# Optimization experiments

Hardware: AMD Instinct MI355X
Metric: run time of the kernel (lower is better)

## Reference

```python
import jax, jax.numpy as jnp
from jax import lax
import numpy as np

H, HKV, D = 16, 4, 128          # query heads, kv heads, head dim
ROT_DIM = 128                    # rotary applied to full head dim
BASE = 10000.0


def rope_cos_sin(S, dtype):
    inv_freq = 1.0 / (BASE ** (jnp.arange(0, ROT_DIM, 2, dtype=jnp.float32) / ROT_DIM))
    t = jnp.arange(S, dtype=jnp.float32)
    freqs = jnp.outer(t, inv_freq)          # (S, ROT_DIM//2)
    return jnp.cos(freqs).astype(dtype), jnp.sin(freqs).astype(dtype)


def apply_rope(x, cos, sin):
    # x: (B, S, h, D); non-interleaved (GPT-NeoX) halves
    d2 = ROT_DIM // 2
    x1, x2 = x[..., :d2], x[..., d2:ROT_DIM]
    c = cos[None, :, None, :]
    s = sin[None, :, None, :]
    rot = jnp.concatenate([x1 * c - x2 * s, x2 * c + x1 * s], axis=-1)
    if ROT_DIM < x.shape[-1]:
        rot = jnp.concatenate([rot, x[..., ROT_DIM:]], axis=-1)
    return rot


def setup_inputs() -> dict:
    key = jax.random.key(0)
    ks = jax.random.split(key, 7)
    B, S, E = 2, 2048, 2048
    qkv_dim = D * (H + 2 * HKV)  # 3072
    return {
        "x": jax.random.normal(ks[0], (B, S, E), jnp.float32),
        "w_in": jax.random.normal(ks[1], (qkv_dim, E), jnp.float32) * (1.0 / np.sqrt(E)),
        "b_in": jax.random.normal(ks[2], (qkv_dim,), jnp.float32) * 0.02,
        "conv_w": jax.random.normal(ks[3], (qkv_dim, 1, 4), jnp.float32) * 0.5,
        "conv_b": jax.random.normal(ks[4], (qkv_dim,), jnp.float32) * 0.02,
        "w_out": jax.random.normal(ks[5], (E, H * D), jnp.float32) * (1.0 / np.sqrt(H * D)),
        "b_out": jax.random.normal(ks[6], (E,), jnp.float32) * 0.02,
    }


def reference(x, w_in, b_in, conv_w, conv_b, w_out, b_out):
    B, S, E = x.shape
    K = conv_w.shape[-1]
    # fused QKV projection
    qkv = x @ w_in.T + b_in                                  # (B, S, 3072)
    # causal depthwise conv1d (torch conv with padding=K-1 then keep first S)
    lhs = jnp.pad(qkv.transpose(0, 2, 1), ((0, 0), (0, 0), (K - 1, 0)))  # (B, C, S+K-1)
    conv = lax.conv_general_dilated(
        lhs, conv_w, (1,), "VALID",
        dimension_numbers=("NCH", "OIH", "NCH"),
        feature_group_count=conv_w.shape[0],
    )
    qkv = (conv + conv_b[None, :, None]).transpose(0, 2, 1)  # (B, S, 3072)
    # split q / kv (GQA)
    q = qkv[..., : H * D].reshape(B, S, H, D)
    kv = qkv[..., H * D :].reshape(B, S, 2, HKV, D)
    cos, sin = rope_cos_sin(S, x.dtype)
    q = apply_rope(q, cos, sin)
    k = apply_rope(kv[:, :, 0], cos, sin)
    v = kv[:, :, 1]
    rep = H // HKV
    k = jnp.repeat(k, rep, axis=2)                           # (B, S, H, D)
    v = jnp.repeat(v, rep, axis=2)
    scale = 1.0 / np.sqrt(D)  # softmax_scale=None -> 1/sqrt(head_dim)
    scores = jnp.einsum("bshd,bthd->bhst", q, k) * scale     # (B, H, S, S)
    causal_mask = jnp.tril(jnp.ones((S, S), bool))
    scores = jnp.where(causal_mask[None, None], scores, jnp.finfo(scores.dtype).min)
    attn = jax.nn.softmax(scores, axis=-1)
    ctx = jnp.einsum("bhst,bthd->bshd", attn, v).reshape(B, S, H * D)
    return ctx @ w_out.T + b_out
```

## Files before the change

kernel.cpp:

```cpp
#include <hip/hip_runtime.h>
#include <type_traits>

#define S_LEN 2048
#define BATCH 2
#define EDIM  2048
#define NH    16
#define NKV   4
#define HDIM  128
#define QKVD  3072
#define QSCALE 0.12751579107188777f

typedef __attribute__((ext_vector_type(8))) short short8;
typedef __attribute__((ext_vector_type(4))) float f32x4;

__device__ __forceinline__ ushort f2bf(float f) {
  union { float f; unsigned u; } un; un.f = f;
  unsigned u = un.u + 0x7fffu + ((un.u >> 16) & 1u);
  return (ushort)(u >> 16);
}
__device__ __forceinline__ float bf2f(ushort h) {
  union { unsigned u; float f; } un; un.u = ((unsigned)h) << 16;
  return un.f;
}
__device__ __forceinline__ unsigned cvt_pk_bf16(float lo, float hi) {
  unsigned r;
  asm("v_cvt_pk_bf16_f32 %0, %1, %2" : "=v"(r) : "v"(lo), "v"(hi));
  return r;
}
__device__ __forceinline__ float fexp2(float x) { return __builtin_amdgcn_exp2f(x); }

__device__ __forceinline__ void load_lds16(const void* g, void* l) {
  __builtin_amdgcn_global_load_lds((const __attribute__((address_space(1))) void*)g,
                                   (__attribute__((address_space(3))) void*)l,
                                   16, 0, 0);
}

__global__ __launch_bounds__(256) void cast3(const float* __restrict__ a,
                                             const float* __restrict__ b,
                                             const float* __restrict__ c,
                                             ushort* __restrict__ oa,
                                             ushort* __restrict__ ob,
                                             ushort* __restrict__ oc) {
  int i = blockIdx.x * 256 + threadIdx.x;
  const float* s; ushort* d; int j;
  if (i < 2097152)      { s = a; d = oa; j = i; }
  else if (i < 3670016) { s = b; d = ob; j = i - 2097152; }
  else                  { s = c; d = oc; j = i - 3670016; }
  float4 v = ((const float4*)s)[j];
  ushort4 o;
  o.x = f2bf(v.x); o.y = f2bf(v.y); o.z = f2bf(v.z); o.w = f2bf(v.w);
  ((ushort4*)d)[j] = o;
}

__global__ __launch_bounds__(256) void transpose_cw(const float* __restrict__ cw,
                                                    float* __restrict__ cwT) {
  int i = blockIdx.x * 256 + threadIdx.x;
  int c = i >> 2, j = i & 3;
  cwT[j * QKVD + c] = cw[i];
}

__global__ __launch_bounds__(256) void rope_table(float* __restrict__ cosT,
                                                  float* __restrict__ sinT) {
  int i = blockIdx.x * 256 + threadIdx.x;
  int s = i >> 6, d = i & 63;
  float inv = expf(-(float)d * 0.14391156831212787f);
  float f = (float)s * inv;
  float sv, cv;
  sincosf(f, &sv, &cv);
  cosT[i] = cv;
  sinT[i] = sv;
}

template <bool OBF>
__global__ __launch_bounds__(256) void gemm_bt(
    const ushort* __restrict__ A, const ushort* __restrict__ Bt,
    const float* __restrict__ bias, void* __restrict__ Cv,
    int M, int N, int K) {
  __shared__ __align__(16) ushort As[128 * 32];
  __shared__ __align__(16) ushort Bs[128 * 32];
  const int tid = threadIdx.x;
  const int wid = tid >> 6, lane = tid & 63;
  const int l15 = lane & 15, lg = lane >> 4;
  const int nTn = N >> 7;
  const int cpx = gridDim.x >> 3;
  const int swz = ((int)blockIdx.x & 7) * cpx + ((int)blockIdx.x >> 3);
  const int m0 = (swz / nTn) * 128, n0 = (swz % nTn) * 128;
  const int wr = (wid >> 1) * 64, wc = (wid & 1) * 64;
  f32x4 acc[4][4] = {};

  for (int k0 = 0; k0 < K; k0 += 32) {
#pragma unroll
    for (int j = 0; j < 2; ++j) {
      const int c = j * 256 + wid * 64 + lane;
      load_lds16(A + (size_t)(m0 + (c >> 2)) * K + k0 + (c & 3) * 8,
                 As + (j * 256 + wid * 64) * 8);
      load_lds16(Bt + (size_t)(n0 + (c >> 2)) * K + k0 + (c & 3) * 8,
                 Bs + (j * 256 + wid * 64) * 8);
    }
    __syncthreads();
    short8 af[4], bf[4];
#pragma unroll
    for (int i = 0; i < 4; i++) {
      af[i] = *(const short8*)&As[(wr + i * 16 + l15) * 32 + lg * 8];
      bf[i] = *(const short8*)&Bs[(wc + i * 16 + l15) * 32 + lg * 8];
    }
#pragma unroll
    for (int mi = 0; mi < 4; mi++)
#pragma unroll
      for (int ni = 0; ni < 4; ni++)
        acc[mi][ni] = __builtin_amdgcn_mfma_f32_16x16x32_bf16(af[mi], bf[ni], acc[mi][ni], 0, 0, 0);
    __syncthreads();
  }

#pragma unroll
  for (int mi = 0; mi < 4; mi++) {
#pragma unroll
    for (int ni = 0; ni < 4; ni++) {
      const int col = n0 + wc + ni * 16 + l15;
      const float bv = bias[col];
#pragma unroll
      for (int r = 0; r < 4; r++) {
        const int row = m0 + wr + mi * 16 + lg * 4 + r;
        if constexpr (OBF)
          ((ushort*)Cv)[(size_t)row * N + col] = f2bf(acc[mi][ni][r] + bv);
        else
          ((float*)Cv)[(size_t)row * N + col] = acc[mi][ni][r] + bv;
      }
    }
  }
}

template <bool OBF>
__global__ __launch_bounds__(512, 2) void gemm256(
    const ushort* __restrict__ A, const ushort* __restrict__ Bt,
    const float* __restrict__ bias, void* __restrict__ Cv,
    int M, int N, int K) {
  __shared__ __align__(16) ushort LA[4][8192];
  __shared__ __align__(16) ushort LB[4][8192];
  const int tid = threadIdx.x;
  const int wid = tid >> 6, lane = tid & 63;
  const int l15 = lane & 15, lg = lane >> 4;
  const int wr = wid >> 2, wc = wid & 3;
  const int nTn = N >> 8;
  const int cpx = gridDim.x >> 3;
  const int swz = ((int)blockIdx.x & 7) * cpx + ((int)blockIdx.x >> 3);
  const int m0 = (swz / nTn) * 256, n0 = (swz % nTn) * 256;
  const ushort* Ag = A + (size_t)m0 * K;
  const ushort* Bg = Bt + (size_t)n0 * K;
  const int coff = (lg ^ ((l15 >> 1) & 3)) * 8;
  const int abase = (wr * 128 + l15) * 32 + coff;
  const int bbase = (wc * 64 + l15) * 32 + coff;
  const int nk = K >> 5;

  f32x4 acc[8][4] = {};

  auto stage_one = [&](const ushort* G, ushort* Ls, int k0) {
#pragma unroll
    for (int i = 0; i < 2; ++i) {
      const int c = i * 512 + tid;
      const int row = c >> 2, cc = c & 3;
      const int scc = cc ^ ((row >> 1) & 3);
      load_lds16(G + (size_t)row * K + k0 + scc * 8,
                 Ls + (i * 512 + wid * 64) * 8);
    }
  };

#pragma unroll
  for (int t = 0; t < 3; ++t) {
    stage_one(Ag, LA[t], t * 32);
    stage_one(Bg, LB[t], t * 32);
  }
  asm volatile("s_waitcnt vmcnt(8)" ::: "memory");
  __builtin_amdgcn_s_barrier();

  auto ktile = [&](auto VMC, auto STG, int t) {
    constexpr int VM = decltype(VMC)::value;
    constexpr bool STAGE = decltype(STG)::value;
    const int slot = t & 3;
    const ushort* Las = LA[slot];
    const ushort* Lbs = LB[slot];
    short8 afr[8], bfr[4];
#pragma unroll
    for (int n = 0; n < 4; ++n) bfr[n] = *(const short8*)&Lbs[bbase + n * 512];
#pragma unroll
    for (int m = 0; m < 8; ++m) afr[m] = *(const short8*)&Las[abase + m * 512];
    if constexpr (STAGE) {
      stage_one(Ag, LA[(t + 3) & 3], (t + 3) * 32);
      stage_one(Bg, LB[(t + 3) & 3], (t + 3) * 32);
    }
    __builtin_amdgcn_s_setprio(1);
#pragma unroll
    for (int m = 0; m < 8; ++m)
#pragma unroll
      for (int n = 0; n < 4; ++n)
        acc[m][n] = __builtin_amdgcn_mfma_f32_16x16x32_bf16(afr[m], bfr[n], acc[m][n], 0, 0, 0);
    __builtin_amdgcn_s_setprio(0);
    if constexpr (VM == 8)      asm volatile("s_waitcnt vmcnt(8)" ::: "memory");
    else if constexpr (VM == 4) asm volatile("s_waitcnt vmcnt(4)" ::: "memory");
    else if constexpr (VM == 0) asm volatile("s_waitcnt vmcnt(0)" ::: "memory");
    __builtin_amdgcn_s_barrier();
  };

  using tru = std::integral_constant<bool, true>;
  using fal = std::integral_constant<bool, false>;
  for (int t = 0; t + 3 < nk; ++t)
    ktile(std::integral_constant<int, 8>{}, tru{}, t);
  ktile(std::integral_constant<int, 4>{}, fal{}, nk - 3);
  ktile(std::integral_constant<int, 0>{}, fal{}, nk - 2);
  ktile(std::integral_constant<int, -1>{}, fal{}, nk - 1);

#pragma unroll
  for (int m = 0; m < 8; ++m)
#pragma unroll
    for (int n = 0; n < 4; ++n) {
      const int col = n0 + wc * 64 + n * 16 + l15;
      const float bv = bias[col];
#pragma unroll
      for (int r = 0; r < 4; ++r) {
        const int row = m0 + wr * 128 + m * 16 + lg * 4 + r;
        if constexpr (OBF)
          ((ushort*)Cv)[(size_t)row * N + col] = f2bf(acc[m][n][r] + bv);
        else
          ((float*)Cv)[(size_t)row * N + col] = acc[m][n][r] + bv;
      }
    }
}

__global__ __launch_bounds__(256) void conv_rope(
    const ushort* __restrict__ qkv, const float* __restrict__ cwT,
    const float* __restrict__ cb, const float* __restrict__ cosT,
    const float* __restrict__ sinT, ushort* __restrict__ Qo,
    ushort* __restrict__ Ko, ushort* __restrict__ Vo) {
  const int token = blockIdx.x;
  const int s = token & (S_LEN - 1);
  const int p = blockIdx.y * 256 + threadIdx.x;

  auto conv4 = [&](int c0, float out[4]) {
    const float4 bb = *(const float4*)&cb[c0];
    out[0] = bb.x; out[1] = bb.y; out[2] = bb.z; out[3] = bb.w;
#pragma unroll
    for (int j = 0; j < 4; j++) {
      int ss = s - 3 + j;
      if (ss >= 0) {
        ushort4 v = *(const ushort4*)&qkv[(size_t)(token - 3 + j) * QKVD + c0];
        const float4 w = *(const float4*)&cwT[j * QKVD + c0];
        out[0] += bf2f(v.x) * w.x;
        out[1] += bf2f(v.y) * w.y;
        out[2] += bf2f(v.z) * w.z;
        out[3] += bf2f(v.w) * w.w;
      }
    }
  };

  if (p < 256) {
    const int h = p >> 4, d0 = (p & 15) * 4;
    const int c1 = h * 128 + d0;
    float x1[4], x2[4];
    conv4(c1, x1); conv4(c1 + 64, x2);
    const float4 co = *(const float4*)&cosT[s * 64 + d0];
    const float4 si = *(const float4*)&sinT[s * 64 + d0];
    ushort4 o1, o2v;
    o1.x = f2bf((x1[0] * co.x - x2[0] * si.x) * QSCALE);
    o1.y = f2bf((x1[1] * co.y - x2[1] * si.y) * QSCALE);
    o1.z = f2bf((x1[2] * co.z - x2[2] * si.z) * QSCALE);
    o1.w = f2bf((x1[3] * co.w - x2[3] * si.w) * QSCALE);
    o2v.x = f2bf((x2[0] * co.x + x1[0] * si.x) * QSCALE);
    o2v.y = f2bf((x2[1] * co.y + x1[1] * si.y) * QSCALE);
    o2v.z = f2bf((x2[2] * co.z + x1[2] * si.z) * QSCALE);
    o2v.w = f2bf((x2[3] * co.w + x1[3] * si.w) * QSCALE);
    const size_t base = ((size_t)token * NH + h) * HDIM + d0;
    *(ushort4*)&Qo[base] = o1;
    *(ushort4*)&Qo[base + 64] = o2v;
  } else if (p < 320) {
    const int idx = p - 256, h = idx >> 4, d0 = (idx & 15) * 4;
    const int c1 = 2048 + h * 128 + d0;
    float x1[4], x2[4];
    conv4(c1, x1); conv4(c1 + 64, x2);
    const float4 co = *(const float4*)&cosT[s * 64 + d0];
    const float4 si = *(const float4*)&sinT[s * 64 + d0];
    ushort4 o1, o2v;
    o1.x = f2bf(x1[0] * co.x - x2[0] * si.x);
    o1.y = f2bf(x1[1] * co.y - x2[1] * si.y);
    o1.z = f2bf(x1[2] * co.z - x2[2] * si.z);
    o1.w = f2bf(x1[3] * co.w - x2[3] * si.w);
    o2v.x = f2bf(x2[0] * co.x + x1[0] * si.x);
    o2v.y = f2bf(x2[1] * co.y + x1[1] * si.y);
    o2v.z = f2bf(x2[2] * co.z + x1[2] * si.z);
    o2v.w = f2bf(x2[3] * co.w + x1[3] * si.w);
    const size_t base = ((size_t)token * NKV + h) * HDIM + d0;
    *(ushort4*)&Ko[base] = o1;
    *(ushort4*)&Ko[base + 64] = o2v;
  } else if (p < 448) {
    const int idx = p - 320;
    const int c0 = 2560 + idx * 4;
    float v[4];
    conv4(c0, v);
    const int hd = idx * 4;
    const int h = hd >> 7, d = hd & 127;
    ushort4 o;
    o.x = f2bf(v[0]); o.y = f2bf(v[1]); o.z = f2bf(v[2]); o.w = f2bf(v[3]);
    *(ushort4*)&Vo[((size_t)token * NKV + h) * HDIM + d] = o;
  }
}

__global__ __launch_bounds__(256) void transpose_v(const ushort* __restrict__ Vb,
                                                   ushort* __restrict__ Vt) {
  __shared__ ushort t[64][65];
  const int tid = threadIdx.x;
  const int s0 = blockIdx.x * 64, d0 = blockIdx.y * 64;
  const int g = blockIdx.z;
  const int b = g >> 2, kvh = g & 3;
#pragma unroll
  for (int p = 0; p < 8; p++) {
    int idx = p * 256 + tid;
    int r = idx >> 5, c2 = (idx & 31) * 2;
    ushort2 v = *(const ushort2*)&Vb[((size_t)(b * S_LEN + s0 + r) * NKV + kvh) * HDIM + d0 + c2];
    t[r][c2] = v.x; t[r][c2 + 1] = v.y;
  }
  __syncthreads();
#pragma unroll
  for (int p = 0; p < 8; p++) {
    int idx = p * 256 + tid;
    int dr = idx >> 5, sc2 = (idx & 31) * 2;
    ushort2 v; v.x = t[sc2][dr]; v.y = t[sc2 + 1][dr];
    *(ushort2*)&Vt[((size_t)g * HDIM + d0 + dr) * S_LEN + s0 + sc2] = v;
  }
}

__global__ __launch_bounds__(256, 3) void attn(
    const ushort* __restrict__ Q, const ushort* __restrict__ K,
    const ushort* __restrict__ Vt, ushort* __restrict__ ctx) {
  __shared__ __align__(16) ushort Ks[2][64 * 128];
  __shared__ __align__(16) ushort Vs[128 * 64];
  const int tid = threadIdx.x;
  const int wid = tid >> 6, lane = tid & 63;
  const int l15 = lane & 15, lg = lane >> 4;
  const int bkv = blockIdx.x;
  const int b = bkv >> 2, kvh = bkv & 3;
  const int h = kvh * 4 + wid;
  const int qb = (gridDim.y - 1) - blockIdx.y;
  const int q0 = qb * 16;

  const ushort* Kbase  = K  + ((size_t)b * S_LEN * NKV + kvh) * HDIM;
  const ushort* Vtbase = Vt + (size_t)bkv * HDIM * S_LEN;

  short8 qf[4];
#pragma unroll
  for (int kd = 0; kd < 4; kd++)
    qf[kd] = *(const short8*)&Q[(((size_t)(b * S_LEN + q0 + l15)) * NH + h) * HDIM + kd * 32 + lg * 8];

  auto stageK = [&](int tile, int bufi) {
    const int j0t = tile * 64;
#pragma unroll
    for (int p = 0; p < 4; ++p) {
      const int i = wid * 4 + p;
      const int row = i * 4 + (lane >> 4);
      const int cs  = (lane & 15) ^ (row & 7);
      load_lds16(Kbase + (size_t)(j0t + row) * (NKV * HDIM) + cs * 8,
                 &Ks[bufi][i * 512]);
    }
  };
  auto stageV = [&](int tile) {
    const int j0t = tile * 64;
#pragma unroll
    for (int p = 0; p < 4; ++p) {
      const int i = wid * 4 + p;
      const int d  = i * 8 + (lane >> 3);
      const int cs = (lane & 7) ^ (d & 7);
      load_lds16(Vtbase + (size_t)d * S_LEN + j0t + cs * 8,
                 &Vs[i * 512]);
    }
  };

  f32x4 o2[8] = {};
  float m_run = -3e30f, l_run = 0.f;
  const int ntile = q0 / 64 + 1;
  const int qrow = q0 + l15;

  stageK(0, 0);
  __syncthreads();
  int buf = 0;
  for (int jt = 0; jt < ntile; ++jt) {
    const int j0 = jt * 64;
    if (jt + 1 < ntile) stageK(jt + 1, buf ^ 1);
    stageV(jt);

    f32x4 sa[4] = {};
#pragma unroll
    for (int t = 0; t < 4; ++t) {
      const int r = t * 16 + l15;
#pragma unroll
      for (int kd = 0; kd < 4; ++kd) {
        short8 kf = *(const short8*)&Ks[buf][r * 128 + (((kd * 4 + lg) ^ (r & 7)) * 8)];
        sa[t] = __builtin_amdgcn_mfma_f32_16x16x32_bf16(kf, qf[kd], sa[t], 0, 0, 0);
      }
    }

    float pv[4][4];
    float mx = -3e30f;
#pragma unroll
    for (int t = 0; t < 4; ++t)
#pragma unroll
      for (int r = 0; r < 4; ++r) {
        float v = sa[t][r];
        if (j0 + t * 16 + lg * 4 + r > qrow) v = -3e30f;
        pv[t][r] = v;
        mx = fmaxf(mx, v);
      }
    mx = fmaxf(mx, __shfl_xor(mx, 16));
    mx = fmaxf(mx, __shfl_xor(mx, 32));
    const float mnew = fmaxf(m_run, mx);
    float sum = 0.f;
#pragma unroll
    for (int t = 0; t < 4; ++t)
#pragma unroll
      for (int r = 0; r < 4; ++r) {
        float p = fexp2(pv[t][r] - mnew);
        pv[t][r] = p;
        sum += p;
      }
    sum += __shfl_xor(sum, 16);
    sum += __shfl_xor(sum, 32);
    const float fac = fexp2(m_run - mnew);
    m_run = mnew;
    l_run = l_run * fac + sum;
#pragma unroll
    for (int dt = 0; dt < 8; ++dt)
#pragma unroll
      for (int r = 0; r < 4; ++r) o2[dt][r] *= fac;

    unsigned pk[4][2];
#pragma unroll
    for (int t = 0; t < 4; ++t)
#pragma unroll
      for (int p = 0; p < 2; ++p)
        pk[t][p] = cvt_pk_bf16(pv[t][2 * p], pv[t][2 * p + 1]);

    union U8 { unsigned u[4]; short8 s; } pfk[2];
#pragma unroll
    for (int ks = 0; ks < 2; ++ks)
#pragma unroll
      for (int j = 0; j < 4; ++j) {
        const int src = ((lg & 1) * 2 + (j >> 1)) * 16 + l15;
        unsigned v0 = __shfl((int)pk[ks * 2][j & 1], src);
        unsigned v1 = __shfl((int)pk[ks * 2 + 1][j & 1], src);
        pfk[ks].u[j] = (lg >= 2) ? v1 : v0;
      }

    __syncthreads();

#pragma unroll
    for (int dt = 0; dt < 8; ++dt) {
      const int d = dt * 16 + l15;
#pragma unroll
      for (int ks = 0; ks < 2; ++ks) {
        short8 vf = *(const short8*)&Vs[d * 64 + (((ks * 4 + lg) ^ (d & 7)) * 8)];
        o2[dt] = __builtin_amdgcn_mfma_f32_16x16x32_bf16(vf, pfk[ks].s, o2[dt], 0, 0, 0);
      }
    }

    __syncthreads();
    buf ^= 1;
  }

  const float inv_l = 1.f / l_run;
  const size_t obase = (((size_t)(b * S_LEN + q0 + l15)) * NH + h) * HDIM;
#pragma unroll
  for (int dt = 0; dt < 8; ++dt) {
    ushort4 w;
    w.x = f2bf(o2[dt][0] * inv_l);
    w.y = f2bf(o2[dt][1] * inv_l);
    w.z = f2bf(o2[dt][2] * inv_l);
    w.w = f2bf(o2[dt][3] * inv_l);
    *(ushort4*)&ctx[obase + dt * 16 + lg * 4] = w;
  }
}

extern "C" void kernel_launch(void* const* d_in, const int* in_sizes, int n_in,
                              void* d_out, int out_size, void* d_ws, size_t ws_size,
                              hipStream_t stream) {
  const float* x      = (const float*)d_in[0];
  const float* w_in   = (const float*)d_in[1];
  const float* b_in   = (const float*)d_in[2];
  const float* conv_w = (const float*)d_in[3];
  const float* conv_b = (const float*)d_in[4];
  const float* w_out  = (const float*)d_in[5];
  const float* b_out  = (const float*)d_in[6];
  float* out = (float*)d_out;

  char* ws = (char*)d_ws;
  size_t off = 0;
  ushort* xbf  = (ushort*)(ws + off); off += (size_t)4096 * 2048 * 2;
  ushort* wibf = (ushort*)(ws + off); off += (size_t)3072 * 2048 * 2;
  ushort* wobf = (ushort*)(ws + off); off += (size_t)2048 * 2048 * 2;
  ushort* qkv  = (ushort*)(ws + off); off += (size_t)4096 * 3072 * 2;
  ushort* Qb   = (ushort*)(ws + off); off += (size_t)4096 * 16 * 128 * 2;
  ushort* Kb   = (ushort*)(ws + off); off += (size_t)4096 * 4 * 128 * 2;
  ushort* Vb   = (ushort*)(ws + off); off += (size_t)4096 * 4 * 128 * 2;
  float*  cosT = (float*)(ws + off);  off += (size_t)2048 * 64 * 4;
  float*  sinT = (float*)(ws + off);  off += (size_t)2048 * 64 * 4;
  float*  cwT  = (float*)(ws + off);  off += (size_t)4 * QKVD * 4;
  ushort* Vtb  = (ushort*)qkv;

  cast3<<<18432, 256, 0, stream>>>(x, w_in, w_out, xbf, wibf, wobf);
  transpose_cw<<<48, 256, 0, stream>>>(conv_w, cwT);
  rope_table<<<512, 256, 0, stream>>>(cosT, sinT);

  gemm256<true><<<192, 512, 0, stream>>>(xbf, wibf, b_in, qkv, 4096, 3072, 2048);
  conv_rope<<<dim3(4096, 2), 256, 0, stream>>>(qkv, cwT, conv_b, cosT, sinT, Qb, Kb, Vb);
  transpose_v<<<dim3(32, 2, 8), 256, 0, stream>>>(Vb, Vtb);
  attn<<<dim3(8, 128), 256, 0, stream>>>(Qb, Kb, Vtb, xbf);
  gemm_bt<false><<<512, 256, 0, stream>>>(xbf, wobf, b_out, out, 4096, 2048, 2048);
}
```

Before: 222.6 us.

## Split long causal attention rows into two KV halves with a combine kernel

```diff
diff --git a/kernel.cpp b/kernel.cpp
--- a/kernel.cpp
+++ b/kernel.cpp
@@ -329,7 +329,8 @@
 
 __global__ __launch_bounds__(256, 3) void attn(
     const ushort* __restrict__ Q, const ushort* __restrict__ K,
-    const ushort* __restrict__ Vt, ushort* __restrict__ ctx) {
+    const ushort* __restrict__ Vt, ushort* __restrict__ ctx,
+    ushort* __restrict__ Pn, float* __restrict__ Ps) {
   __shared__ __align__(16) ushort Ks[2][64 * 128];
   __shared__ __align__(16) ushort Vs[128 * 64];
   const int tid = threadIdx.x;
@@ -338,7 +339,18 @@
   const int bkv = blockIdx.x;
   const int b = bkv >> 2, kvh = bkv & 3;
   const int h = kvh * 4 + wid;
-  const int qb = (gridDim.y - 1) - blockIdx.y;
+  const int y = blockIdx.y;
+  int qb, jtlo, jthi, half;
+  bool split;
+  if (y < 128) {
+    split = true; qb = 127 - (y >> 1); half = y & 1;
+    const int nt = qb / 4 + 1, mid = nt >> 1;
+    jtlo = half ? mid : 0;
+    jthi = half ? nt : mid;
+  } else {
+    split = false; qb = 191 - y; half = 0;
+    jtlo = 0; jthi = qb / 4 + 1;
+  }
   const int q0 = qb * 16;
 
   const ushort* Kbase  = K  + ((size_t)b * S_LEN * NKV + kvh) * HDIM;
@@ -374,15 +386,14 @@
 
   f32x4 o2[8] = {};
   float m_run = -3e30f, l_run = 0.f;
-  const int ntile = q0 / 64 + 1;
   const int qrow = q0 + l15;
 
-  stageK(0, 0);
+  stageK(jtlo, 0);
   __syncthreads();
   int buf = 0;
-  for (int jt = 0; jt < ntile; ++jt) {
+  for (int jt = jtlo; jt < jthi; ++jt) {
     const int j0 = jt * 64;
-    if (jt + 1 < ntile) stageK(jt + 1, buf ^ 1);
+    if (jt + 1 < jthi) stageK(jt + 1, buf ^ 1);
     stageV(jt);
 
     f32x4 sa[4] = {};
@@ -464,16 +475,65 @@
   }
 
   const float inv_l = 1.f / l_run;
-  const size_t obase = (((size_t)(b * S_LEN + q0 + l15)) * NH + h) * HDIM;
-#pragma unroll
-  for (int dt = 0; dt < 8; ++dt) {
-    ushort4 w;
-    w.x = f2bf(o2[dt][0] * inv_l);
-    w.y = f2bf(o2[dt][1] * inv_l);
-    w.z = f2bf(o2[dt][2] * inv_l);
-    w.w = f2bf(o2[dt][3] * inv_l);
-    *(ushort4*)&ctx[obase + dt * 16 + lg * 4] = w;
-  }
+  if (!split) {
+    const size_t obase = (((size_t)(b * S_LEN + q0 + l15)) * NH + h) * HDIM;
+#pragma unroll
+    for (int dt = 0; dt < 8; ++dt) {
+      ushort4 w;
+      w.x = f2bf(o2[dt][0] * inv_l);
+      w.y = f2bf(o2[dt][1] * inv_l);
+      w.z = f2bf(o2[dt][2] * inv_l);
+      w.w = f2bf(o2[dt][3] * inv_l);
+      *(ushort4*)&ctx[obase + dt * 16 + lg * 4] = w;
+    }
+  } else {
+    const int R = ((bkv * 64 + (qb - 64)) * 2 + half) * 4 + wid;
+    if (lg == 0) Ps[R * 16 + l15] = m_run + __log2f(l_run);
+    const size_t pbase = ((size_t)R * 16 + l15) * HDIM;
+#pragma unroll
+    for (int dt = 0; dt < 8; ++dt) {
+      ushort4 w;
+      w.x = f2bf(o2[dt][0] * inv_l);
+      w.y = f2bf(o2[dt][1] * inv_l);
+      w.z = f2bf(o2[dt][2] * inv_l);
+      w.w = f2bf(o2[dt][3] * inv_l);
+      *(ushort4*)&Pn[pbase + dt * 16 + lg * 4] = w;
+    }
+  }
+}
+
+__global__ __launch_bounds__(256) void combine(const ushort* __restrict__ Pn,
+                                               const float* __restrict__ Ps,
+                                               ushort* __restrict__ ctx) {
+  const int g = blockIdx.x * 256 + threadIdx.x;
+  const int seg = g & 15, r = g >> 4;
+  const int q = r & 15, hh = (r >> 4) & 3, qb64 = (r >> 6) & 63, bkv = r >> 12;
+  const int base2 = (bkv * 64 + qb64) * 2;
+  const int R0 = (base2 + 0) * 4 + hh, R1 = (base2 + 1) * 4 + hh;
+  const float s0 = Ps[R0 * 16 + q], s1 = Ps[R1 * 16 + q];
+  const float sm = fmaxf(s0, s1);
+  float w0 = fexp2(s0 - sm), w1 = fexp2(s1 - sm);
+  const float inv = 1.f / (w0 + w1);
+  w0 *= inv; w1 *= inv;
+  const int d0 = seg * 8;
+  const ushort* p0 = &Pn[((size_t)R0 * 16 + q) * HDIM + d0];
+  const ushort* p1 = &Pn[((size_t)R1 * 16 + q) * HDIM + d0];
+  const int token = (bkv >> 2) * S_LEN + 1024 + qb64 * 16 + q;
+  const int head = (bkv & 3) * 4 + hh;
+  ushort* o = &ctx[((size_t)token * NH + head) * HDIM + d0];
+  ushort4 a0 = *(const ushort4*)p0, b0 = *(const ushort4*)(p0 + 4);
+  ushort4 a1 = *(const ushort4*)p1, b1 = *(const ushort4*)(p1 + 4);
+  ushort4 r0, r1;
+  r0.x = f2bf(bf2f(a0.x) * w0 + bf2f(a1.x) * w1);
+  r0.y = f2bf(bf2f(a0.y) * w0 + bf2f(a1.y) * w1);
+  r0.z = f2bf(bf2f(a0.z) * w0 + bf2f(a1.z) * w1);
+  r0.w = f2bf(bf2f(a0.w) * w0 + bf2f(a1.w) * w1);
+  r1.x = f2bf(bf2f(b0.x) * w0 + bf2f(b1.x) * w1);
+  r1.y = f2bf(bf2f(b0.y) * w0 + bf2f(b1.y) * w1);
+  r1.z = f2bf(bf2f(b0.z) * w0 + bf2f(b1.z) * w1);
+  r1.w = f2bf(bf2f(b0.w) * w0 + bf2f(b1.w) * w1);
+  *(ushort4*)o = r0;
+  *(ushort4*)(o + 4) = r1;
 }
 
 extern "C" void kernel_launch(void* const* d_in, const int* in_sizes, int n_in,
@@ -500,6 +560,8 @@
   float*  cosT = (float*)(ws + off);  off += (size_t)2048 * 64 * 4;
   float*  sinT = (float*)(ws + off);  off += (size_t)2048 * 64 * 4;
   float*  cwT  = (float*)(ws + off);  off += (size_t)4 * QKVD * 4;
+  ushort* Pn   = (ushort*)(ws + off); off += (size_t)8 * 64 * 2 * 4 * 16 * 128 * 2;
+  float*  Ps   = (float*)(ws + off);  off += (size_t)8 * 64 * 2 * 4 * 16 * 4;
   ushort* Vtb  = (ushort*)qkv;
 
   cast3<<<18432, 256, 0, stream>>>(x, w_in, w_out, xbf, wibf, wobf);
@@ -509,6 +571,7 @@
   gemm256<true><<<192, 512, 0, stream>>>(xbf, wibf, b_in, qkv, 4096, 3072, 2048);
   conv_rope<<<dim3(4096, 2), 256, 0, stream>>>(qkv, cwT, conv_b, cosT, sinT, Qb, Kb, Vb);
   transpose_v<<<dim3(32, 2, 8), 256, 0, stream>>>(Vb, Vtb);
-  attn<<<dim3(8, 128), 256, 0, stream>>>(Qb, Kb, Vtb, xbf);
+  attn<<<dim3(8, 192), 256, 0, stream>>>(Qb, Kb, Vtb, xbf, Pn, Ps);
+  combine<<<2048, 256, 0, stream>>>(Pn, Ps, xbf);
   gemm_bt<false><<<512, 256, 0, stream>>>(xbf, wobf, b_out, out, 4096, 2048, 2048);
 }
```

New measurement: 234.3 us. 5.3% more time.

## Pipeline output GEMM with 4-slot LDS prefetch and swizzled layout

Applied to the files above, without the earlier changes.

```diff
diff --git a/kernel.cpp b/kernel.cpp
--- a/kernel.cpp
+++ b/kernel.cpp
@@ -72,62 +72,99 @@
 }
 
 template <bool OBF>
-__global__ __launch_bounds__(256) void gemm_bt(
+__global__ __launch_bounds__(256, 2) void gemm128(
     const ushort* __restrict__ A, const ushort* __restrict__ Bt,
     const float* __restrict__ bias, void* __restrict__ Cv,
     int M, int N, int K) {
-  __shared__ __align__(16) ushort As[128 * 32];
-  __shared__ __align__(16) ushort Bs[128 * 32];
+  __shared__ __align__(16) ushort LA[4][4096];
+  __shared__ __align__(16) ushort LB[4][4096];
   const int tid = threadIdx.x;
   const int wid = tid >> 6, lane = tid & 63;
   const int l15 = lane & 15, lg = lane >> 4;
+  const int wr = wid >> 1, wc = wid & 1;
   const int nTn = N >> 7;
   const int cpx = gridDim.x >> 3;
   const int swz = ((int)blockIdx.x & 7) * cpx + ((int)blockIdx.x >> 3);
   const int m0 = (swz / nTn) * 128, n0 = (swz % nTn) * 128;
-  const int wr = (wid >> 1) * 64, wc = (wid & 1) * 64;
+  const ushort* Ag = A + (size_t)m0 * K;
+  const ushort* Bg = Bt + (size_t)n0 * K;
+  const int coff = (lg ^ ((l15 >> 1) & 3)) * 8;
+  const int abase = (wr * 64 + l15) * 32 + coff;
+  const int bbase = (wc * 64 + l15) * 32 + coff;
+  const int nk = K >> 5;
+
   f32x4 acc[4][4] = {};
 
-  for (int k0 = 0; k0 < K; k0 += 32) {
-#pragma unroll
-    for (int j = 0; j < 2; ++j) {
-      const int c = j * 256 + wid * 64 + lane;
-      load_lds16(A + (size_t)(m0 + (c >> 2)) * K + k0 + (c & 3) * 8,
-                 As + (j * 256 + wid * 64) * 8);
-      load_lds16(Bt + (size_t)(n0 + (c >> 2)) * K + k0 + (c & 3) * 8,
-                 Bs + (j * 256 + wid * 64) * 8);
-    }
-    __syncthreads();
-    short8 af[4], bf[4];
-#pragma unroll
-    for (int i = 0; i < 4; i++) {
-      af[i] = *(const short8*)&As[(wr + i * 16 + l15) * 32 + lg * 8];
-      bf[i] = *(const short8*)&Bs[(wc + i * 16 + l15) * 32 + lg * 8];
-    }
-#pragma unroll
-    for (int mi = 0; mi < 4; mi++)
-#pragma unroll
-      for (int ni = 0; ni < 4; ni++)
-        acc[mi][ni] = __builtin_amdgcn_mfma_f32_16x16x32_bf16(af[mi], bf[ni], acc[mi][ni], 0, 0, 0);
-    __syncthreads();
-  }
-
-#pragma unroll
-  for (int mi = 0; mi < 4; mi++) {
-#pragma unroll
-    for (int ni = 0; ni < 4; ni++) {
-      const int col = n0 + wc + ni * 16 + l15;
+  auto stage_one = [&](const ushort* G, ushort* Ls, int k0) {
+#pragma unroll
+    for (int i = 0; i < 2; ++i) {
+      const int c = i * 256 + tid;
+      const int row = c >> 2, cc = c & 3;
+      const int scc = cc ^ ((row >> 1) & 3);
+      load_lds16(G + (size_t)row * K + k0 + scc * 8,
+                 Ls + (i * 256 + wid * 64) * 8);
+    }
+  };
+
+#pragma unroll
+  for (int t = 0; t < 3; ++t) {
+    stage_one(Ag, LA[t], t * 32);
+    stage_one(Bg, LB[t], t * 32);
+  }
+  asm volatile("s_waitcnt vmcnt(8)" ::: "memory");
+  __builtin_amdgcn_s_barrier();
+
+  auto ktile = [&](auto VMC, auto STG, int t) {
+    constexpr int VM = decltype(VMC)::value;
+    constexpr bool STAGE = decltype(STG)::value;
+    const int slot = t & 3;
+    const ushort* Las = LA[slot];
+    const ushort* Lbs = LB[slot];
+    short8 afr[4], bfr[4];
+#pragma unroll
+    for (int n = 0; n < 4; ++n) bfr[n] = *(const short8*)&Lbs[bbase + n * 512];
+#pragma unroll
+    for (int m = 0; m < 4; ++m) afr[m] = *(const short8*)&Las[abase + m * 512];
+    if constexpr (STAGE) {
+      stage_one(Ag, LA[(t + 3) & 3], (t + 3) * 32);
+      stage_one(Bg, LB[(t + 3) & 3], (t + 3) * 32);
+    }
+    __builtin_amdgcn_s_setprio(1);
+#pragma unroll
+    for (int m = 0; m < 4; ++m)
+#pragma unroll
+      for (int n = 0; n < 4; ++n)
+        acc[m][n] = __builtin_amdgcn_mfma_f32_16x16x32_bf16(afr[m], bfr[n], acc[m][n], 0, 0, 0);
+    __builtin_amdgcn_s_setprio(0);
+    if constexpr (VM == 8)      asm volatile("s_waitcnt vmcnt(8)" ::: "memory");
+    else if constexpr (VM == 4) asm volatile("s_waitcnt vmcnt(4)" ::: "memory");
+    else if constexpr (VM == 0) asm volatile("s_waitcnt vmcnt(0)" ::: "memory");
+    __builtin_amdgcn_s_barrier();
+  };
+
+  using tru = std::integral_constant<bool, true>;
+  using fal = std::integral_constant<bool, false>;
+  for (int t = 0; t + 3 < nk; ++t)
+    ktile(std::integral_constant<int, 8>{}, tru{}, t);
+  ktile(std::integral_constant<int, 4>{}, fal{}, nk - 3);
+  ktile(std::integral_constant<int, 0>{}, fal{}, nk - 2);
+  ktile(std::integral_constant<int, -1>{}, fal{}, nk - 1);
+
+#pragma unroll
+  for (int m = 0; m < 4; ++m)
+#pragma unroll
+    for (int n = 0; n < 4; ++n) {
+      const int col = n0 + wc * 64 + n * 16 + l15;
       const float bv = bias[col];
 #pragma unroll
-      for (int r = 0; r < 4; r++) {
-        const int row = m0 + wr + mi * 16 + lg * 4 + r;
+      for (int r = 0; r < 4; ++r) {
+        const int row = m0 + wr * 64 + m * 16 + lg * 4 + r;
         if constexpr (OBF)
-          ((ushort*)Cv)[(size_t)row * N + col] = f2bf(acc[mi][ni][r] + bv);
+          ((ushort*)Cv)[(size_t)row * N + col] = f2bf(acc[m][n][r] + bv);
         else
-          ((float*)Cv)[(size_t)row * N + col] = acc[mi][ni][r] + bv;
-      }
-    }
-  }
+          ((float*)Cv)[(size_t)row * N + col] = acc[m][n][r] + bv;
+      }
+    }
 }
 
 template <bool OBF>
@@ -510,5 +547,5 @@
   conv_rope<<<dim3(4096, 2), 256, 0, stream>>>(qkv, cwT, conv_b, cosT, sinT, Qb, Kb, Vb);
   transpose_v<<<dim3(32, 2, 8), 256, 0, stream>>>(Vb, Vtb);
   attn<<<dim3(8, 128), 256, 0, stream>>>(Qb, Kb, Vtb, xbf);
-  gemm_bt<false><<<512, 256, 0, stream>>>(xbf, wobf, b_out, out, 4096, 2048, 2048);
-}
+  gemm128<false><<<512, 256, 0, stream>>>(xbf, wobf, b_out, out, 4096, 2048, 2048);
+}
```

After: 210.3 us. -5.5%, faster.
